# Performance work log

Measured on AMD Instinct MI355X. Metric: run time of the kernel, lower is better.

The kernel has to match this reference:

```python
import jax, jax.numpy as jnp
import numpy as np

N_NODES = 50000
N_EDGES = 800000
IN_FEATURES = 256
HIDDEN = 128


def setup_inputs() -> dict:
    key = jax.random.key(0)
    k_x, k_r, k_c, k_v, k_w, k_b = jax.random.split(key, 6)
    x = jax.random.normal(k_x, (N_NODES, IN_FEATURES), dtype=jnp.float32)
    adj_row = jax.random.randint(k_r, (N_EDGES,), 0, N_NODES, dtype=jnp.int32)
    adj_col = jax.random.randint(k_c, (N_EDGES,), 0, N_NODES, dtype=jnp.int32)
    adj_val = jax.random.uniform(k_v, (N_EDGES,), dtype=jnp.float32)
    # Linear params: weight [hidden, in_features] (xavier-normal-ish), bias [hidden]
    std = float(np.sqrt(2.0 / (IN_FEATURES + HIDDEN)))
    W = jax.random.normal(k_w, (HIDDEN, IN_FEATURES), dtype=jnp.float32) * std
    b = jax.random.normal(k_b, (HIDDEN,), dtype=jnp.float32) * 0.01
    return {"x": x, "adj_row": adj_row, "adj_col": adj_col, "adj_val": adj_val, "W": W, "b": b}


def reference(x, adj_row, adj_col, adj_val, W, b):
    # support = Linear(x): [N, hidden]
    support = jnp.einsum('nf,hf->nh', x, W) + b
    # sparse adj @ support via edge-list gather + segment-sum scatter
    gathered = support[adj_col] * adj_val[:, None]          # [E, hidden]
    out = jax.ops.segment_sum(gathered, adj_row, num_segments=N_NODES)  # [N, hidden]
    return out
```

## Files before the change

kernel.cpp:

```cpp
#include <hip/hip_runtime.h>

#define N_NODES 50000
#define N_EDGES 800000
#define IN_F    256
#define HIDDEN  128

#define BUCKET_SZ 64
#define NB        782
#define NBP       1024
#define EBLOCK    2048
#define EBLOCKS   391
#define CAP       1344
#define OV_CAP    4096

typedef __attribute__((ext_vector_type(8))) short bf16x8;
typedef __attribute__((ext_vector_type(4))) float f32x4;

__device__ inline unsigned short f2bf(float f) {
    unsigned u = __float_as_uint(f);
    u += 0x7FFF + ((u >> 16) & 1);
    return (unsigned short)(u >> 16);
}
__device__ inline bf16x8 cvt8(float4 a, float4 b) {
    bf16x8 r;
    r[0] = (short)f2bf(a.x); r[1] = (short)f2bf(a.y);
    r[2] = (short)f2bf(a.z); r[3] = (short)f2bf(a.w);
    r[4] = (short)f2bf(b.x); r[5] = (short)f2bf(b.y);
    r[6] = (short)f2bf(b.z); r[7] = (short)f2bf(b.w);
    return r;
}
__device__ inline float bfLo(unsigned u) { return __uint_as_float(u << 16); }
__device__ inline float bfHi(unsigned u) { return __uint_as_float(u & 0xFFFF0000u); }

__global__ __launch_bounds__(256) void linear_mfma_kernel(
    const float* __restrict__ x, const float* __restrict__ W,
    const float* __restrict__ bias, unsigned short* __restrict__ support)
{
    __shared__ __align__(16) short wfrag[8 * 8 * 64 * 8];

    const int tid = threadIdx.x;
#pragma unroll
    for (int it = 0; it < 16; ++it) {
        const int f    = it * 256 + tid;
        const int ln   = f & 63;
        const int s    = (f >> 6) & 7;
        const int kc   = f >> 9;
        const int row  = s * 16 + (ln & 15);
        const int k0   = kc * 32 + (ln >> 4) * 8;
        const float* wp = W + (size_t)row * IN_F + k0;
        float4 b0 = *(const float4*)wp;
        float4 b1 = *(const float4*)(wp + 4);
        *(bf16x8*)(&wfrag[(size_t)f * 8]) = cvt8(b0, b1);
    }
    __syncthreads();

    const int lane = tid & 63;
    const int wave = tid >> 6;
    const int quad = lane >> 4;
    const int l16  = lane & 15;

    int m = blockIdx.x * 64 + wave * 16 + l16;
    if (m >= N_NODES) m = N_NODES - 1;
    const float* xrow = x + (size_t)m * IN_F;

    f32x4 acc[8];
#pragma unroll
    for (int s = 0; s < 8; ++s) acc[s] = (f32x4){0.f, 0.f, 0.f, 0.f};

#pragma unroll
    for (int kc = 0; kc < 8; ++kc) {
        const int k0 = kc * 32 + quad * 8;
        float4 a0 = *(const float4*)(xrow + k0);
        float4 a1 = *(const float4*)(xrow + k0 + 4);
        bf16x8 af = cvt8(a0, a1);
        const short* bbase = &wfrag[((size_t)(kc * 8) * 64 + lane) * 8];
#pragma unroll
        for (int s = 0; s < 8; ++s) {
            bf16x8 bf = *(const bf16x8*)(bbase + (size_t)s * 64 * 8);
            acc[s] = __builtin_amdgcn_mfma_f32_16x16x32_bf16(af, bf, acc[s], 0, 0, 0);
        }
    }

    const int rowBase = blockIdx.x * 64 + wave * 16 + quad * 4;
#pragma unroll
    for (int reg = 0; reg < 4; ++reg) {
        const int r = rowBase + reg;
        if (r < N_NODES) {
#pragma unroll
            for (int s = 0; s < 8; ++s) {
                const int col = s * 16 + l16;
                float v = acc[s][reg] + bias[col];
                support[(size_t)r * HIDDEN + col] = f2bf(v);
            }
        }
    }
}

__global__ __launch_bounds__(256) void partition_kernel(
    const int* __restrict__ adj_row, const int* __restrict__ adj_col,
    const float* __restrict__ adj_val, int* __restrict__ cursor,
    int2* __restrict__ part, int4* __restrict__ ovbuf, int* __restrict__ ovcnt)
{
    __shared__ int  lcnt[NBP];
    __shared__ int  lcur[NBP];
    __shared__ int  gbase[NBP];
    __shared__ int  tsum[256];
    __shared__ int2 lbuf[EBLOCK];

    const int tid  = threadIdx.x;
    const int base = blockIdx.x * EBLOCK;
    const int n    = min(EBLOCK, N_EDGES - base);

    for (int i = tid; i < NBP; i += 256) lcnt[i] = 0;
    __syncthreads();

    unsigned pk[8]; float pv[8];
#pragma unroll
    for (int i = 0; i < 8; ++i) {
        int e = base + tid + i * 256;
        bool ok = e < N_EDGES;
        int ee = ok ? e : 0;
        int r = adj_row[ee], c = adj_col[ee];
        float v = adj_val[ee];
        if (ok) {
            unsigned bk = (unsigned)r >> 6;
            pk[i] = (bk << 22) | (((unsigned)r & 63u) << 16) | (unsigned)c;
            pv[i] = v;
            atomicAdd(&lcnt[bk], 1);
        } else pk[i] = 0xFFFFFFFFu;
    }
    __syncthreads();

    int s0 = lcnt[tid * 4], s1 = lcnt[tid * 4 + 1];
    int s2 = lcnt[tid * 4 + 2], s3 = lcnt[tid * 4 + 3];
    int mysum = s0 + s1 + s2 + s3;
    tsum[tid] = mysum;
    __syncthreads();
#pragma unroll
    for (int off = 1; off < 256; off <<= 1) {
        int t = (tid >= off) ? tsum[tid - off] : 0;
        __syncthreads();
        tsum[tid] += t;
        __syncthreads();
    }
    int ex = tsum[tid] - mysum;
    lcnt[tid * 4]     = ex;
    lcnt[tid * 4 + 1] = ex + s0;
    lcnt[tid * 4 + 2] = ex + s0 + s1;
    lcnt[tid * 4 + 3] = ex + s0 + s1 + s2;
    __syncthreads();

    for (int b = tid; b < NB; b += 256) {
        int c = lcnt[b + 1] - lcnt[b];
        gbase[b] = (c > 0) ? atomicAdd(&cursor[b], c) : 0;
        lcur[b]  = lcnt[b];
    }
    __syncthreads();

#pragma unroll
    for (int i = 0; i < 8; ++i) {
        if (pk[i] != 0xFFFFFFFFu) {
            unsigned bk = pk[i] >> 22;
            int p = atomicAdd(&lcur[bk], 1);
            lbuf[p] = make_int2((int)pk[i], __float_as_int(pv[i]));
        }
    }
    __syncthreads();

    for (int j = tid; j < n; j += 256) {
        int2 cv = lbuf[j];
        unsigned bk = ((unsigned)cv.x) >> 22;
        int loc = gbase[bk] + (j - lcnt[bk]);
        if (loc < CAP) {
            part[(size_t)bk * CAP + loc] = make_int2(cv.x & 0x3FFFFF, cv.y);
        } else {
            int op = atomicAdd(ovcnt, 1);
            if (op < OV_CAP) {
                int r = (int)(bk * BUCKET_SZ) + ((cv.x >> 16) & 63);
                ovbuf[op] = make_int4(r, cv.x & 0xFFFF, cv.y, 0);
            }
        }
    }
}

__global__ __launch_bounds__(256) void bucket_gather_kernel(
    const int* __restrict__ cursor, const int2* __restrict__ part,
    const unsigned int* __restrict__ support_u32, float* __restrict__ out)
{
    __shared__ int2 sbuf[CAP];
    __shared__ int  hist[BUCKET_SZ];
    __shared__ int  rp[BUCKET_SZ + 1];
    __shared__ int  cur[BUCKET_SZ];

    const int tid  = threadIdx.x;
    const int b    = blockIdx.x;
    const int n    = min(cursor[b], CAP);
    const int wave = tid >> 6;
    const int lane = tid & 63;

    if (tid < BUCKET_SZ) hist[tid] = 0;
    __syncthreads();

    int2 held[(CAP + 255) / 256];
    int  nheld = 0;
    const int2* pb = part + (size_t)b * CAP;
    for (int j = tid; j < n; j += 256) {
        int2 cv = pb[j];
        held[nheld++] = cv;
        atomicAdd(&hist[(cv.x >> 16) & 63], 1);
    }
    __syncthreads();

    if (tid < 64) {
        int v = hist[tid];
        int incl = v;
#pragma unroll
        for (int off = 1; off < 64; off <<= 1) {
            int t = __shfl_up(incl, off);
            if (tid >= off) incl += t;
        }
        rp[tid + 1] = incl;
        if (tid == 0) rp[0] = 0;
        cur[tid] = incl - v;
    }
    __syncthreads();

    for (int i = 0; i < nheld; ++i) {
        int r = (held[i].x >> 16) & 63;
        int p = atomicAdd(&cur[r], 1);
        sbuf[p] = held[i];
    }
    __syncthreads();

    const int rowLo = wave * 16;
#pragma unroll 1
    for (int r = rowLo; r < rowLo + 16; ++r) {
        const int grow = b * BUCKET_SZ + r;
        if (grow >= N_NODES) break;
        const int s = rp[r], e = rp[r + 1];
        float ax = 0.f, ay = 0.f;
        int j = s;
        for (; j + 3 < e; j += 4) {
            int2 c0 = sbuf[j],     c1 = sbuf[j + 1];
            int2 c2 = sbuf[j + 2], c3 = sbuf[j + 3];
            unsigned u0 = support_u32[(size_t)(c0.x & 0xFFFF) * 64 + lane];
            unsigned u1 = support_u32[(size_t)(c1.x & 0xFFFF) * 64 + lane];
            unsigned u2 = support_u32[(size_t)(c2.x & 0xFFFF) * 64 + lane];
            unsigned u3 = support_u32[(size_t)(c3.x & 0xFFFF) * 64 + lane];
            float v0 = __int_as_float(c0.y), v1 = __int_as_float(c1.y);
            float v2 = __int_as_float(c2.y), v3 = __int_as_float(c3.y);
            ax += v0 * bfLo(u0); ay += v0 * bfHi(u0);
            ax += v1 * bfLo(u1); ay += v1 * bfHi(u1);
            ax += v2 * bfLo(u2); ay += v2 * bfHi(u2);
            ax += v3 * bfLo(u3); ay += v3 * bfHi(u3);
        }
        for (; j < e; ++j) {
            int2 cv = sbuf[j];
            unsigned u = support_u32[(size_t)(cv.x & 0xFFFF) * 64 + lane];
            float v = __int_as_float(cv.y);
            ax += v * bfLo(u); ay += v * bfHi(u);
        }
        *(float2*)(out + (size_t)grow * HIDDEN + lane * 2) = make_float2(ax, ay);
    }
}

__global__ __launch_bounds__(256) void overflow_fix_kernel(
    const int* __restrict__ ovcnt, const int4* __restrict__ ovbuf,
    const unsigned int* __restrict__ support_u32, float* __restrict__ out)
{
    const int n    = min(*ovcnt, OV_CAP);
    const int wave = threadIdx.x >> 6;
    const int lane = threadIdx.x & 63;
    for (int j = wave; j < n; j += 4) {
        int4 o = ovbuf[j];
        unsigned u = support_u32[(size_t)o.y * 64 + lane];
        float v = __int_as_float(o.z);
        unsafeAtomicAdd(out + (size_t)o.x * HIDDEN + lane * 2,     v * bfLo(u));
        unsafeAtomicAdd(out + (size_t)o.x * HIDDEN + lane * 2 + 1, v * bfHi(u));
    }
}

extern "C" void kernel_launch(void* const* d_in, const int* in_sizes, int n_in,
                              void* d_out, int out_size, void* d_ws, size_t ws_size,
                              hipStream_t stream) {
    const float* x       = (const float*)d_in[0];
    const int*   adj_row = (const int*)d_in[1];
    const int*   adj_col = (const int*)d_in[2];
    const float* adj_val = (const float*)d_in[3];
    const float* W       = (const float*)d_in[4];
    const float* b       = (const float*)d_in[5];
    float* out = (float*)d_out;

    char* wsb = (char*)d_ws;
    const size_t off_support = 0;
    const size_t off_part    = off_support + (size_t)N_NODES * HIDDEN * 2;
    const size_t off_cursor  = off_part + (size_t)NB * CAP * 8;
    const size_t off_ovcnt   = off_cursor + (size_t)NB * 4;
    const size_t off_ovbuf   = (off_ovcnt + 4 + 15) & ~(size_t)15;

    unsigned short* support = (unsigned short*)(wsb + off_support);
    int2* part   = (int2*)(wsb + off_part);
    int*  cursor = (int*)(wsb + off_cursor);
    int*  ovcnt  = (int*)(wsb + off_ovcnt);
    int4* ovbuf  = (int4*)(wsb + off_ovbuf);

    hipMemsetAsync(cursor, 0, (size_t)(NB + 1) * 4, stream);

    linear_mfma_kernel<<<(N_NODES + 63) / 64, 256, 0, stream>>>(x, W, b, support);
    partition_kernel<<<EBLOCKS, 256, 0, stream>>>(
        adj_row, adj_col, adj_val, cursor, part, ovbuf, ovcnt);
    bucket_gather_kernel<<<NB, 256, 0, stream>>>(
        cursor, part, (const unsigned int*)support, out);
    overflow_fix_kernel<<<1, 256, 0, stream>>>(
        ovcnt, ovbuf, (const unsigned int*)support, out);
}
```

Baseline: 192.8 us.

## Fuse linear GEMM with edge partition and widen gather buckets to 128 rows

The MFMA linear kernel and the edge partition kernel now share one launch, with block index picking the role, so the two independent stages can overlap and one launch is dropped. Shared memory is unified at 32KB, so the weight fragment is staged in two halves with extra barriers. Buckets grow from 64 to 128 rows with a larger per-bucket capacity, and the gather kernel runs 512 threads per bucket with a two-segment scan. Fewer and larger buckets reduce global cursor atomics but change occupancy and load balance in the gather stage.

Measured after the change: 187.0 us. 3.0% less time.

```diff
diff --git a/kernel.cpp b/kernel.cpp
--- a/kernel.cpp
+++ b/kernel.cpp
@@ -5,12 +5,13 @@
 #define IN_F    256
 #define HIDDEN  128
 
-#define BUCKET_SZ 64
-#define NB        782
-#define NBP       1024
+#define BUCKET_SZ 128
+#define NB        391
+#define NBS       512
 #define EBLOCK    2048
 #define EBLOCKS   391
-#define CAP       1344
+#define LBLOCKS   782
+#define CAP       2500
 #define OV_CAP    4096
 
 typedef __attribute__((ext_vector_type(8))) short bf16x8;
@@ -32,158 +33,162 @@
 __device__ inline float bfLo(unsigned u) { return __uint_as_float(u << 16); }
 __device__ inline float bfHi(unsigned u) { return __uint_as_float(u & 0xFFFF0000u); }
 
-__global__ __launch_bounds__(256) void linear_mfma_kernel(
+__global__ __launch_bounds__(256) void fused_linear_partition_kernel(
     const float* __restrict__ x, const float* __restrict__ W,
-    const float* __restrict__ bias, unsigned short* __restrict__ support)
-{
-    __shared__ __align__(16) short wfrag[8 * 8 * 64 * 8];
-
-    const int tid = threadIdx.x;
-#pragma unroll
-    for (int it = 0; it < 16; ++it) {
-        const int f    = it * 256 + tid;
-        const int ln   = f & 63;
-        const int s    = (f >> 6) & 7;
-        const int kc   = f >> 9;
-        const int row  = s * 16 + (ln & 15);
-        const int k0   = kc * 32 + (ln >> 4) * 8;
-        const float* wp = W + (size_t)row * IN_F + k0;
-        float4 b0 = *(const float4*)wp;
-        float4 b1 = *(const float4*)(wp + 4);
-        *(bf16x8*)(&wfrag[(size_t)f * 8]) = cvt8(b0, b1);
-    }
-    __syncthreads();
-
-    const int lane = tid & 63;
-    const int wave = tid >> 6;
-    const int quad = lane >> 4;
-    const int l16  = lane & 15;
-
-    int m = blockIdx.x * 64 + wave * 16 + l16;
-    if (m >= N_NODES) m = N_NODES - 1;
-    const float* xrow = x + (size_t)m * IN_F;
-
-    f32x4 acc[8];
-#pragma unroll
-    for (int s = 0; s < 8; ++s) acc[s] = (f32x4){0.f, 0.f, 0.f, 0.f};
-
-#pragma unroll
-    for (int kc = 0; kc < 8; ++kc) {
-        const int k0 = kc * 32 + quad * 8;
-        float4 a0 = *(const float4*)(xrow + k0);
-        float4 a1 = *(const float4*)(xrow + k0 + 4);
-        bf16x8 af = cvt8(a0, a1);
-        const short* bbase = &wfrag[((size_t)(kc * 8) * 64 + lane) * 8];
-#pragma unroll
-        for (int s = 0; s < 8; ++s) {
-            bf16x8 bf = *(const bf16x8*)(bbase + (size_t)s * 64 * 8);
-            acc[s] = __builtin_amdgcn_mfma_f32_16x16x32_bf16(af, bf, acc[s], 0, 0, 0);
-        }
-    }
-
-    const int rowBase = blockIdx.x * 64 + wave * 16 + quad * 4;
-#pragma unroll
-    for (int reg = 0; reg < 4; ++reg) {
-        const int r = rowBase + reg;
-        if (r < N_NODES) {
-#pragma unroll
-            for (int s = 0; s < 8; ++s) {
-                const int col = s * 16 + l16;
-                float v = acc[s][reg] + bias[col];
-                support[(size_t)r * HIDDEN + col] = f2bf(v);
-            }
-        }
-    }
-}
-
-__global__ __launch_bounds__(256) void partition_kernel(
+    const float* __restrict__ bias, unsigned short* __restrict__ support,
     const int* __restrict__ adj_row, const int* __restrict__ adj_col,
     const float* __restrict__ adj_val, int* __restrict__ cursor,
     int2* __restrict__ part, int4* __restrict__ ovbuf, int* __restrict__ ovcnt)
 {
-    __shared__ int  lcnt[NBP];
-    __shared__ int  lcur[NBP];
-    __shared__ int  gbase[NBP];
-    __shared__ int  tsum[256];
-    __shared__ int2 lbuf[EBLOCK];
-
-    const int tid  = threadIdx.x;
-    const int base = blockIdx.x * EBLOCK;
-    const int n    = min(EBLOCK, N_EDGES - base);
-
-    for (int i = tid; i < NBP; i += 256) lcnt[i] = 0;
-    __syncthreads();
-
-    unsigned pk[8]; float pv[8];
-#pragma unroll
-    for (int i = 0; i < 8; ++i) {
-        int e = base + tid + i * 256;
-        bool ok = e < N_EDGES;
-        int ee = ok ? e : 0;
-        int r = adj_row[ee], c = adj_col[ee];
-        float v = adj_val[ee];
-        if (ok) {
-            unsigned bk = (unsigned)r >> 6;
-            pk[i] = (bk << 22) | (((unsigned)r & 63u) << 16) | (unsigned)c;
-            pv[i] = v;
-            atomicAdd(&lcnt[bk], 1);
-        } else pk[i] = 0xFFFFFFFFu;
-    }
-    __syncthreads();
-
-    int s0 = lcnt[tid * 4], s1 = lcnt[tid * 4 + 1];
-    int s2 = lcnt[tid * 4 + 2], s3 = lcnt[tid * 4 + 3];
-    int mysum = s0 + s1 + s2 + s3;
-    tsum[tid] = mysum;
-    __syncthreads();
-#pragma unroll
-    for (int off = 1; off < 256; off <<= 1) {
-        int t = (tid >= off) ? tsum[tid - off] : 0;
-        __syncthreads();
-        tsum[tid] += t;
-        __syncthreads();
-    }
-    int ex = tsum[tid] - mysum;
-    lcnt[tid * 4]     = ex;
-    lcnt[tid * 4 + 1] = ex + s0;
-    lcnt[tid * 4 + 2] = ex + s0 + s1;
-    lcnt[tid * 4 + 3] = ex + s0 + s1 + s2;
-    __syncthreads();
-
-    for (int b = tid; b < NB; b += 256) {
-        int c = lcnt[b + 1] - lcnt[b];
-        gbase[b] = (c > 0) ? atomicAdd(&cursor[b], c) : 0;
-        lcur[b]  = lcnt[b];
-    }
-    __syncthreads();
-
-#pragma unroll
-    for (int i = 0; i < 8; ++i) {
-        if (pk[i] != 0xFFFFFFFFu) {
-            unsigned bk = pk[i] >> 22;
-            int p = atomicAdd(&lcur[bk], 1);
-            lbuf[p] = make_int2((int)pk[i], __float_as_int(pv[i]));
-        }
-    }
-    __syncthreads();
-
-    for (int j = tid; j < n; j += 256) {
-        int2 cv = lbuf[j];
-        unsigned bk = ((unsigned)cv.x) >> 22;
-        int loc = gbase[bk] + (j - lcnt[bk]);
-        if (loc < CAP) {
-            part[(size_t)bk * CAP + loc] = make_int2(cv.x & 0x3FFFFF, cv.y);
-        } else {
-            int op = atomicAdd(ovcnt, 1);
-            if (op < OV_CAP) {
-                int r = (int)(bk * BUCKET_SZ) + ((cv.x >> 16) & 63);
-                ovbuf[op] = make_int4(r, cv.x & 0xFFFF, cv.y, 0);
-            }
-        }
-    }
-}
-
-__global__ __launch_bounds__(256) void bucket_gather_kernel(
+    __shared__ __align__(16) char smem[32768];
+    const int tid = threadIdx.x;
+
+    if (blockIdx.x < EBLOCKS) {
+        int2* lbuf  = (int2*)smem;
+        int*  lofs  = (int*)(smem + 16384);
+        int*  lcur  = (int*)(smem + 18432);
+        int*  gbase = (int*)(smem + 20480);
+        int*  tsum  = (int*)(smem + 22528);
+
+        const int base = blockIdx.x * EBLOCK;
+        const int n    = min(EBLOCK, N_EDGES - base);
+
+        for (int i = tid; i < NBS; i += 256) lofs[i] = 0;
+        __syncthreads();
+
+        unsigned pk[8]; float pv[8];
+#pragma unroll
+        for (int i = 0; i < 8; ++i) {
+            int e = base + tid + i * 256;
+            bool ok = e < N_EDGES;
+            int ee = ok ? e : 0;
+            int r = adj_row[ee], c = adj_col[ee];
+            float v = adj_val[ee];
+            if (ok) {
+                unsigned bk = (unsigned)r >> 7;
+                pk[i] = (bk << 23) | (((unsigned)r & 127u) << 16) | (unsigned)c;
+                pv[i] = v;
+                atomicAdd(&lofs[bk], 1);
+            } else pk[i] = 0xFFFFFFFFu;
+        }
+        __syncthreads();
+
+        int s0 = lofs[tid * 2], s1 = lofs[tid * 2 + 1];
+        int mysum = s0 + s1;
+        tsum[tid] = mysum;
+        __syncthreads();
+#pragma unroll
+        for (int off = 1; off < 256; off <<= 1) {
+            int t = (tid >= off) ? tsum[tid - off] : 0;
+            __syncthreads();
+            tsum[tid] += t;
+            __syncthreads();
+        }
+        int ex = tsum[tid] - mysum;
+        lofs[tid * 2]     = ex;
+        lofs[tid * 2 + 1] = ex + s0;
+        __syncthreads();
+
+        for (int b = tid; b < NB; b += 256) {
+            int nb2 = (b * 2 + 2 < NBS) ? lofs[b + 1] : n;
+            int c = lofs[b + 1] - lofs[b];
+            (void)nb2;
+            gbase[b] = (c > 0) ? atomicAdd(&cursor[b], c) : 0;
+            lcur[b]  = lofs[b];
+        }
+        __syncthreads();
+
+#pragma unroll
+        for (int i = 0; i < 8; ++i) {
+            if (pk[i] != 0xFFFFFFFFu) {
+                unsigned bk = pk[i] >> 23;
+                int p = atomicAdd(&lcur[bk], 1);
+                lbuf[p] = make_int2((int)pk[i], __float_as_int(pv[i]));
+            }
+        }
+        __syncthreads();
+
+        for (int j = tid; j < n; j += 256) {
+            int2 cv = lbuf[j];
+            unsigned bk = ((unsigned)cv.x) >> 23;
+            int loc = gbase[bk] + (j - lofs[bk]);
+            if (loc < CAP) {
+                part[(size_t)bk * CAP + loc] = make_int2(cv.x & 0x7FFFFF, cv.y);
+            } else {
+                int op = atomicAdd(ovcnt, 1);
+                if (op < OV_CAP) {
+                    int r = (int)(bk * BUCKET_SZ) + ((cv.x >> 16) & 127);
+                    ovbuf[op] = make_int4(r, cv.x & 0xFFFF, cv.y, 0);
+                }
+            }
+        }
+    } else {
+        short* wfrag = (short*)smem;
+
+        const int bid  = blockIdx.x - EBLOCKS;
+        const int lane = tid & 63;
+        const int wave = tid >> 6;
+        const int quad = lane >> 4;
+        const int l16  = lane & 15;
+
+        int m = bid * 64 + wave * 16 + l16;
+        if (m >= N_NODES) m = N_NODES - 1;
+        const float* xrow = x + (size_t)m * IN_F;
+
+        f32x4 acc[8];
+#pragma unroll
+        for (int s = 0; s < 8; ++s) acc[s] = (f32x4){0.f, 0.f, 0.f, 0.f};
+
+#pragma unroll
+        for (int half = 0; half < 2; ++half) {
+#pragma unroll
+            for (int it = 0; it < 8; ++it) {
+                const int f   = it * 256 + tid;
+                const int ln  = f & 63;
+                const int s   = (f >> 6) & 7;
+                const int kc  = f >> 9;
+                const int row = s * 16 + (ln & 15);
+                const int k0  = (half * 4 + kc) * 32 + (ln >> 4) * 8;
+                const float* wp = W + (size_t)row * IN_F + k0;
+                float4 b0 = *(const float4*)wp;
+                float4 b1 = *(const float4*)(wp + 4);
+                *(bf16x8*)(&wfrag[(size_t)f * 8]) = cvt8(b0, b1);
+            }
+            __syncthreads();
+
+#pragma unroll
+            for (int kc = 0; kc < 4; ++kc) {
+                const int k0 = (half * 4 + kc) * 32 + quad * 8;
+                float4 a0 = *(const float4*)(xrow + k0);
+                float4 a1 = *(const float4*)(xrow + k0 + 4);
+                bf16x8 af = cvt8(a0, a1);
+                const short* bbase = &wfrag[((size_t)(kc * 8) * 64 + lane) * 8];
+#pragma unroll
+                for (int s = 0; s < 8; ++s) {
+                    bf16x8 bf = *(const bf16x8*)(bbase + (size_t)s * 64 * 8);
+                    acc[s] = __builtin_amdgcn_mfma_f32_16x16x32_bf16(af, bf, acc[s], 0, 0, 0);
+                }
+            }
+            __syncthreads();
+        }
+
+        const int rowBase = bid * 64 + wave * 16 + quad * 4;
+#pragma unroll
+        for (int reg = 0; reg < 4; ++reg) {
+            const int r = rowBase + reg;
+            if (r < N_NODES) {
+#pragma unroll
+                for (int s = 0; s < 8; ++s) {
+                    const int col = s * 16 + l16;
+                    float v = acc[s][reg] + bias[col];
+                    support[(size_t)r * HIDDEN + col] = f2bf(v);
+                }
+            }
+        }
+    }
+}
+
+__global__ __launch_bounds__(512) void bucket_gather_kernel(
     const int* __restrict__ cursor, const int2* __restrict__ part,
     const unsigned int* __restrict__ support_u32, float* __restrict__ out)
 {
@@ -201,32 +206,36 @@
     if (tid < BUCKET_SZ) hist[tid] = 0;
     __syncthreads();
 
-    int2 held[(CAP + 255) / 256];
+    int2 held[(CAP + 511) / 512];
     int  nheld = 0;
     const int2* pb = part + (size_t)b * CAP;
-    for (int j = tid; j < n; j += 256) {
+    for (int j = tid; j < n; j += 512) {
         int2 cv = pb[j];
         held[nheld++] = cv;
-        atomicAdd(&hist[(cv.x >> 16) & 63], 1);
+        atomicAdd(&hist[(cv.x >> 16) & 127], 1);
     }
     __syncthreads();
 
     if (tid < 64) {
-        int v = hist[tid];
-        int incl = v;
+        int a = hist[tid], c = hist[tid + 64];
+        int ia = a, ic = c;
 #pragma unroll
         for (int off = 1; off < 64; off <<= 1) {
-            int t = __shfl_up(incl, off);
-            if (tid >= off) incl += t;
-        }
-        rp[tid + 1] = incl;
+            int ta = __shfl_up(ia, off);
+            int tc = __shfl_up(ic, off);
+            if (tid >= off) { ia += ta; ic += tc; }
+        }
+        int totA = __shfl(ia, 63);
+        rp[tid + 1]      = ia;
+        rp[tid + 65]     = totA + ic;
         if (tid == 0) rp[0] = 0;
-        cur[tid] = incl - v;
+        cur[tid]      = ia - a;
+        cur[tid + 64] = totA + ic - c;
     }
     __syncthreads();
 
     for (int i = 0; i < nheld; ++i) {
-        int r = (held[i].x >> 16) & 63;
+        int r = (held[i].x >> 16) & 127;
         int p = atomicAdd(&cur[r], 1);
         sbuf[p] = held[i];
     }
@@ -306,10 +315,9 @@
 
     hipMemsetAsync(cursor, 0, (size_t)(NB + 1) * 4, stream);
 
-    linear_mfma_kernel<<<(N_NODES + 63) / 64, 256, 0, stream>>>(x, W, b, support);
-    partition_kernel<<<EBLOCKS, 256, 0, stream>>>(
-        adj_row, adj_col, adj_val, cursor, part, ovbuf, ovcnt);
-    bucket_gather_kernel<<<NB, 256, 0, stream>>>(
+    fused_linear_partition_kernel<<<EBLOCKS + LBLOCKS, 256, 0, stream>>>(
+        x, W, b, support, adj_row, adj_col, adj_val, cursor, part, ovbuf, ovcnt);
+    bucket_gather_kernel<<<NB, 512, 0, stream>>>(
         cursor, part, (const unsigned int*)support, out);
     overflow_fix_kernel<<<1, 256, 0, stream>>>(
         ovcnt, ovbuf, (const unsigned int*)support, out);
```

## Fuse linear GEMM and edge partition into one launch, widen gather blocks

Applied to the files above, without the earlier changes.

Merges the MFMA linear kernel and the edge-partition kernel into one launch, with blockIdx deciding the role, so the two independent phases run at the same time and one launch is dropped. The linear branch now stages W in two halves through a 32KB shared buffer to cut LDS use, and prefetches the next x chunk before each MFMA step. The gather kernel goes from 256 to 512 threads per bucket, 8 rows per wave, for more memory-level parallelism. The risks are extra syncs and W reloads in the GEMM path, and heterogeneous blocks in one grid.

Measured after the change: 187.2 us. 2.9% less time.

```diff
diff --git a/kernel.cpp b/kernel.cpp
--- a/kernel.cpp
+++ b/kernel.cpp
@@ -10,6 +10,7 @@
 #define NBP       1024
 #define EBLOCK    2048
 #define EBLOCKS   391
+#define LBLOCKS   782
 #define CAP       1344
 #define OV_CAP    4096
 
@@ -32,158 +33,169 @@
 __device__ inline float bfLo(unsigned u) { return __uint_as_float(u << 16); }
 __device__ inline float bfHi(unsigned u) { return __uint_as_float(u & 0xFFFF0000u); }
 
-__global__ __launch_bounds__(256) void linear_mfma_kernel(
+__global__ __launch_bounds__(256) void fused_linear_partition_kernel(
     const float* __restrict__ x, const float* __restrict__ W,
-    const float* __restrict__ bias, unsigned short* __restrict__ support)
-{
-    __shared__ __align__(16) short wfrag[8 * 8 * 64 * 8];
-
-    const int tid = threadIdx.x;
-#pragma unroll
-    for (int it = 0; it < 16; ++it) {
-        const int f    = it * 256 + tid;
-        const int ln   = f & 63;
-        const int s    = (f >> 6) & 7;
-        const int kc   = f >> 9;
-        const int row  = s * 16 + (ln & 15);
-        const int k0   = kc * 32 + (ln >> 4) * 8;
-        const float* wp = W + (size_t)row * IN_F + k0;
-        float4 b0 = *(const float4*)wp;
-        float4 b1 = *(const float4*)(wp + 4);
-        *(bf16x8*)(&wfrag[(size_t)f * 8]) = cvt8(b0, b1);
-    }
-    __syncthreads();
-
-    const int lane = tid & 63;
-    const int wave = tid >> 6;
-    const int quad = lane >> 4;
-    const int l16  = lane & 15;
-
-    int m = blockIdx.x * 64 + wave * 16 + l16;
-    if (m >= N_NODES) m = N_NODES - 1;
-    const float* xrow = x + (size_t)m * IN_F;
-
-    f32x4 acc[8];
-#pragma unroll
-    for (int s = 0; s < 8; ++s) acc[s] = (f32x4){0.f, 0.f, 0.f, 0.f};
-
-#pragma unroll
-    for (int kc = 0; kc < 8; ++kc) {
-        const int k0 = kc * 32 + quad * 8;
-        float4 a0 = *(const float4*)(xrow + k0);
-        float4 a1 = *(const float4*)(xrow + k0 + 4);
-        bf16x8 af = cvt8(a0, a1);
-        const short* bbase = &wfrag[((size_t)(kc * 8) * 64 + lane) * 8];
-#pragma unroll
-        for (int s = 0; s < 8; ++s) {
-            bf16x8 bf = *(const bf16x8*)(bbase + (size_t)s * 64 * 8);
-            acc[s] = __builtin_amdgcn_mfma_f32_16x16x32_bf16(af, bf, acc[s], 0, 0, 0);
-        }
-    }
-
-    const int rowBase = blockIdx.x * 64 + wave * 16 + quad * 4;
-#pragma unroll
-    for (int reg = 0; reg < 4; ++reg) {
-        const int r = rowBase + reg;
-        if (r < N_NODES) {
-#pragma unroll
-            for (int s = 0; s < 8; ++s) {
-                const int col = s * 16 + l16;
-                float v = acc[s][reg] + bias[col];
-                support[(size_t)r * HIDDEN + col] = f2bf(v);
-            }
-        }
-    }
-}
-
-__global__ __launch_bounds__(256) void partition_kernel(
+    const float* __restrict__ bias, unsigned short* __restrict__ support,
     const int* __restrict__ adj_row, const int* __restrict__ adj_col,
     const float* __restrict__ adj_val, int* __restrict__ cursor,
     int2* __restrict__ part, int4* __restrict__ ovbuf, int* __restrict__ ovcnt)
 {
-    __shared__ int  lcnt[NBP];
-    __shared__ int  lcur[NBP];
-    __shared__ int  gbase[NBP];
-    __shared__ int  tsum[256];
-    __shared__ int2 lbuf[EBLOCK];
-
-    const int tid  = threadIdx.x;
-    const int base = blockIdx.x * EBLOCK;
-    const int n    = min(EBLOCK, N_EDGES - base);
-
-    for (int i = tid; i < NBP; i += 256) lcnt[i] = 0;
-    __syncthreads();
-
-    unsigned pk[8]; float pv[8];
-#pragma unroll
-    for (int i = 0; i < 8; ++i) {
-        int e = base + tid + i * 256;
-        bool ok = e < N_EDGES;
-        int ee = ok ? e : 0;
-        int r = adj_row[ee], c = adj_col[ee];
-        float v = adj_val[ee];
-        if (ok) {
-            unsigned bk = (unsigned)r >> 6;
-            pk[i] = (bk << 22) | (((unsigned)r & 63u) << 16) | (unsigned)c;
-            pv[i] = v;
-            atomicAdd(&lcnt[bk], 1);
-        } else pk[i] = 0xFFFFFFFFu;
-    }
-    __syncthreads();
-
-    int s0 = lcnt[tid * 4], s1 = lcnt[tid * 4 + 1];
-    int s2 = lcnt[tid * 4 + 2], s3 = lcnt[tid * 4 + 3];
-    int mysum = s0 + s1 + s2 + s3;
-    tsum[tid] = mysum;
-    __syncthreads();
-#pragma unroll
-    for (int off = 1; off < 256; off <<= 1) {
-        int t = (tid >= off) ? tsum[tid - off] : 0;
-        __syncthreads();
-        tsum[tid] += t;
-        __syncthreads();
-    }
-    int ex = tsum[tid] - mysum;
-    lcnt[tid * 4]     = ex;
-    lcnt[tid * 4 + 1] = ex + s0;
-    lcnt[tid * 4 + 2] = ex + s0 + s1;
-    lcnt[tid * 4 + 3] = ex + s0 + s1 + s2;
-    __syncthreads();
-
-    for (int b = tid; b < NB; b += 256) {
-        int c = lcnt[b + 1] - lcnt[b];
-        gbase[b] = (c > 0) ? atomicAdd(&cursor[b], c) : 0;
-        lcur[b]  = lcnt[b];
-    }
-    __syncthreads();
-
-#pragma unroll
-    for (int i = 0; i < 8; ++i) {
-        if (pk[i] != 0xFFFFFFFFu) {
-            unsigned bk = pk[i] >> 22;
-            int p = atomicAdd(&lcur[bk], 1);
-            lbuf[p] = make_int2((int)pk[i], __float_as_int(pv[i]));
-        }
-    }
-    __syncthreads();
-
-    for (int j = tid; j < n; j += 256) {
-        int2 cv = lbuf[j];
-        unsigned bk = ((unsigned)cv.x) >> 22;
-        int loc = gbase[bk] + (j - lcnt[bk]);
-        if (loc < CAP) {
-            part[(size_t)bk * CAP + loc] = make_int2(cv.x & 0x3FFFFF, cv.y);
-        } else {
-            int op = atomicAdd(ovcnt, 1);
-            if (op < OV_CAP) {
-                int r = (int)(bk * BUCKET_SZ) + ((cv.x >> 16) & 63);
-                ovbuf[op] = make_int4(r, cv.x & 0xFFFF, cv.y, 0);
-            }
-        }
-    }
-}
-
-__global__ __launch_bounds__(256) void bucket_gather_kernel(
+    __shared__ __align__(16) char smem[32768];
+    const int tid = threadIdx.x;
+
+    if (blockIdx.x < EBLOCKS) {
+        int2* lbuf  = (int2*)smem;
+        int*  lcnt  = (int*)(smem + 16384);
+        int*  lcur  = (int*)(smem + 20480);
+        int*  gbase = (int*)(smem + 24576);
+        int*  tsum  = (int*)(smem + 28672);
+
+        const int base = blockIdx.x * EBLOCK;
+        const int n    = min(EBLOCK, N_EDGES - base);
+
+        for (int i = tid; i < NBP; i += 256) lcnt[i] = 0;
+        __syncthreads();
+
+        unsigned pk[8]; float pv[8];
+#pragma unroll
+        for (int i = 0; i < 8; ++i) {
+            int e = base + tid + i * 256;
+            bool ok = e < N_EDGES;
+            int ee = ok ? e : 0;
+            int r = adj_row[ee], c = adj_col[ee];
+            float v = adj_val[ee];
+            if (ok) {
+                unsigned bk = (unsigned)r >> 6;
+                pk[i] = (bk << 22) | (((unsigned)r & 63u) << 16) | (unsigned)c;
+                pv[i] = v;
+                atomicAdd(&lcnt[bk], 1);
+            } else pk[i] = 0xFFFFFFFFu;
+        }
+        __syncthreads();
+
+        int s0 = lcnt[tid * 4], s1 = lcnt[tid * 4 + 1];
+        int s2 = lcnt[tid * 4 + 2], s3 = lcnt[tid * 4 + 3];
+        int mysum = s0 + s1 + s2 + s3;
+        tsum[tid] = mysum;
+        __syncthreads();
+#pragma unroll
+        for (int off = 1; off < 256; off <<= 1) {
+            int t = (tid >= off) ? tsum[tid - off] : 0;
+            __syncthreads();
+            tsum[tid] += t;
+            __syncthreads();
+        }
+        int ex = tsum[tid] - mysum;
+        lcnt[tid * 4]     = ex;
+        lcnt[tid * 4 + 1] = ex + s0;
+        lcnt[tid * 4 + 2] = ex + s0 + s1;
+        lcnt[tid * 4 + 3] = ex + s0 + s1 + s2;
+        __syncthreads();
+
+        for (int b = tid; b < NB; b += 256) {
+            int c = lcnt[b + 1] - lcnt[b];
+            gbase[b] = (c > 0) ? atomicAdd(&cursor[b], c) : 0;
+            lcur[b]  = lcnt[b];
+        }
+        __syncthreads();
+
+#pragma unroll
+        for (int i = 0; i < 8; ++i) {
+            if (pk[i] != 0xFFFFFFFFu) {
+                unsigned bk = pk[i] >> 22;
+                int p = atomicAdd(&lcur[bk], 1);
+                lbuf[p] = make_int2((int)pk[i], __float_as_int(pv[i]));
+            }
+        }
+        __syncthreads();
+
+        for (int j = tid; j < n; j += 256) {
+            int2 cv = lbuf[j];
+            unsigned bk = ((unsigned)cv.x) >> 22;
+            int loc = gbase[bk] + (j - lcnt[bk]);
+            if (loc < CAP) {
+                part[(size_t)bk * CAP + loc] = make_int2(cv.x & 0x3FFFFF, cv.y);
+            } else {
+                int op = atomicAdd(ovcnt, 1);
+                if (op < OV_CAP) {
+                    int r = (int)(bk * BUCKET_SZ) + ((cv.x >> 16) & 63);
+                    ovbuf[op] = make_int4(r, cv.x & 0xFFFF, cv.y, 0);
+                }
+            }
+        }
+    } else {
+        short* wfrag = (short*)smem;
+
+        const int bid  = blockIdx.x - EBLOCKS;
+        const int lane = tid & 63;
+        const int wave = tid >> 6;
+        const int quad = lane >> 4;
+        const int l16  = lane & 15;
+
+        int m = bid * 64 + wave * 16 + l16;
+        if (m >= N_NODES) m = N_NODES - 1;
+        const float* xrow = x + (size_t)m * IN_F;
+
+        f32x4 acc[8];
+#pragma unroll
+        for (int s = 0; s < 8; ++s) acc[s] = (f32x4){0.f, 0.f, 0.f, 0.f};
+
+        float4 a0 = *(const float4*)(xrow + quad * 8);
+        float4 a1 = *(const float4*)(xrow + quad * 8 + 4);
+
+#pragma unroll
+        for (int half = 0; half < 2; ++half) {
+#pragma unroll
+            for (int it = 0; it < 8; ++it) {
+                const int f   = it * 256 + tid;
+                const int ln  = f & 63;
+                const int s   = (f >> 6) & 7;
+                const int kc  = f >> 9;
+                const int row = s * 16 + (ln & 15);
+                const int k0  = (half * 4 + kc) * 32 + (ln >> 4) * 8;
+                const float* wp = W + (size_t)row * IN_F + k0;
+                float4 b0 = *(const float4*)wp;
+                float4 b1 = *(const float4*)(wp + 4);
+                *(bf16x8*)(&wfrag[(size_t)f * 8]) = cvt8(b0, b1);
+            }
+            __syncthreads();
+
+#pragma unroll
+            for (int kc = 0; kc < 4; ++kc) {
+                const int g = half * 4 + kc;
+                bf16x8 af = cvt8(a0, a1);
+                if (g < 7) {
+                    const int k1 = (g + 1) * 32 + quad * 8;
+                    a0 = *(const float4*)(xrow + k1);
+                    a1 = *(const float4*)(xrow + k1 + 4);
+                }
+                const short* bbase = &wfrag[((size_t)(kc * 8) * 64 + lane) * 8];
+#pragma unroll
+                for (int s = 0; s < 8; ++s) {
+                    bf16x8 bf = *(const bf16x8*)(bbase + (size_t)s * 64 * 8);
+                    acc[s] = __builtin_amdgcn_mfma_f32_16x16x32_bf16(af, bf, acc[s], 0, 0, 0);
+                }
+            }
+            __syncthreads();
+        }
+
+        const int rowBase = bid * 64 + wave * 16 + quad * 4;
+#pragma unroll
+        for (int reg = 0; reg < 4; ++reg) {
+            const int r = rowBase + reg;
+            if (r < N_NODES) {
+#pragma unroll
+                for (int s = 0; s < 8; ++s) {
+                    const int col = s * 16 + l16;
+                    float v = acc[s][reg] + bias[col];
+                    support[(size_t)r * HIDDEN + col] = f2bf(v);
+                }
+            }
+        }
+    }
+}
+
+__global__ __launch_bounds__(512) void bucket_gather_kernel(
     const int* __restrict__ cursor, const int2* __restrict__ part,
     const unsigned int* __restrict__ support_u32, float* __restrict__ out)
 {
@@ -201,10 +213,10 @@
     if (tid < BUCKET_SZ) hist[tid] = 0;
     __syncthreads();
 
-    int2 held[(CAP + 255) / 256];
+    int2 held[(CAP + 511) / 512];
     int  nheld = 0;
     const int2* pb = part + (size_t)b * CAP;
-    for (int j = tid; j < n; j += 256) {
+    for (int j = tid; j < n; j += 512) {
         int2 cv = pb[j];
         held[nheld++] = cv;
         atomicAdd(&hist[(cv.x >> 16) & 63], 1);
@@ -232,9 +244,9 @@
     }
     __syncthreads();
 
-    const int rowLo = wave * 16;
+    const int rowLo = wave * 8;
 #pragma unroll 1
-    for (int r = rowLo; r < rowLo + 16; ++r) {
+    for (int r = rowLo; r < rowLo + 8; ++r) {
         const int grow = b * BUCKET_SZ + r;
         if (grow >= N_NODES) break;
         const int s = rp[r], e = rp[r + 1];
@@ -306,10 +318,9 @@
 
     hipMemsetAsync(cursor, 0, (size_t)(NB + 1) * 4, stream);
 
-    linear_mfma_kernel<<<(N_NODES + 63) / 64, 256, 0, stream>>>(x, W, b, support);
-    partition_kernel<<<EBLOCKS, 256, 0, stream>>>(
-        adj_row, adj_col, adj_val, cursor, part, ovbuf, ovcnt);
-    bucket_gather_kernel<<<NB, 256, 0, stream>>>(
+    fused_linear_partition_kernel<<<EBLOCKS + LBLOCKS, 256, 0, stream>>>(
+        x, W, b, support, adj_row, adj_col, adj_val, cursor, part, ovbuf, ovcnt);
+    bucket_gather_kernel<<<NB, 512, 0, stream>>>(
         cursor, part, (const unsigned int*)support, out);
     overflow_fix_kernel<<<1, 256, 0, stream>>>(
         ovcnt, ovbuf, (const unsigned int*)support, out);
```
